# Optimization experiments

Measured on AMD Instinct MI355X. Metric: run time of the kernel, lower is better.

Reference implementation:

```python
import jax, jax.numpy as jnp
import numpy as np

B, L, D, V, O = 512, 256, 256, 100000, 1000  # L must equal D (see MaxPool1d(kernel_size=D) + squeeze)


def setup_inputs() -> dict:
    key = jax.random.key(0)
    k1, k2, k3, k4, k5 = jax.random.split(key, 5)
    input_sentence = jax.random.randint(k1, (B, L), 0, V)
    emb_weight = jax.random.normal(k2, (V, D), dtype=jnp.float32) * 0.02
    # xavier_uniform for W_b: bound = sqrt(6/(D+D))
    bound = float(np.sqrt(6.0 / (D + D)))
    W_b = jax.random.uniform(k3, (D, D), dtype=jnp.float32, minval=-bound, maxval=bound)
    lw = float(np.sqrt(1.0 / D))
    lin_w = jax.random.uniform(k4, (O, D), dtype=jnp.float32, minval=-lw, maxval=lw)
    lin_b = jax.random.uniform(k5, (O,), dtype=jnp.float32, minval=-lw, maxval=lw)
    return {"input_sentence": input_sentence, "emb_weight": emb_weight,
            "W_b": W_b, "lin_w": lin_w, "lin_b": lin_b}


def reference(input_sentence, emb_weight, W_b, lin_w, lin_b):
    # Embedding lookup: [B, L, D]
    we = emb_weight[input_sentence]
    # torch stores embeddings as [B, D, L] then re-transposes inside the co-attention;
    # net effect: C = tanh(E W_b E^T) with E = [B, L, D]  ->  C: [B, L, L]
    C = jnp.tanh(jnp.einsum('bld,de,bme->blm', we, W_b, we))
    # Dropout(p=0.5) is identity in eval mode.
    # MaxPool1d(kernel_size=D) over last axis with L == D -> max over last dim, keepdims
    max_cow = jnp.max(C, axis=-1, keepdims=True)          # [B, L, 1]
    a_q = jax.nn.softmax(max_cow, axis=1)                  # softmax over L
    # bmm(a_q^T [B,1,L], E [B,L,D]) -> [B,1,D], then squeeze dim 1
    f_w = jnp.einsum('blo,bld->bod', a_q, we)[:, 0, :]     # [B, D]
    return f_w @ lin_w.T + lin_b                           # [B, O]
```

## Files before the change

### kernel.cpp

```cpp
#include <hip/hip_runtime.h>
#include <hip/hip_bf16.h>
#include <math.h>

#define B_ 512
#define L_ 256
#define D_ 256
#define V_ 100000
#define O_ 1000

typedef __attribute__((ext_vector_type(8))) short short8;
typedef __attribute__((ext_vector_type(4))) float f32x4;

static __device__ __forceinline__ unsigned short f2bf(float f) {
    union { float f; unsigned u; } v; v.f = f;
    unsigned r = v.u + 0x7FFFu + ((v.u >> 16) & 1u);
    return (unsigned short)(r >> 16);
}
static __device__ __forceinline__ float bf2f(unsigned short u) {
    union { unsigned u; float f; } v; v.u = ((unsigned)u) << 16;
    return v.f;
}
static __device__ __forceinline__ short8 pack8(float4 a, float4 c) {
    short8 o;
    o[0] = (short)f2bf(a.x); o[1] = (short)f2bf(a.y);
    o[2] = (short)f2bf(a.z); o[3] = (short)f2bf(a.w);
    o[4] = (short)f2bf(c.x); o[5] = (short)f2bf(c.y);
    o[6] = (short)f2bf(c.z); o[7] = (short)f2bf(c.w);
    return o;
}
static __device__ __forceinline__ int fsw(int d) { return d ^ (((d >> 5) & 7) << 2); }

__global__ __launch_bounds__(256) void k_wt(const float* __restrict__ Wb,
                                            unsigned short* __restrict__ Wbf) {
    int i = blockIdx.x * 256 + threadIdx.x;
    Wbf[i] = f2bf(Wb[i]);
}

__global__ __launch_bounds__(1024, 4) void k_attn(const int* __restrict__ tok,
                                                  const float* __restrict__ emb,
                                                  const unsigned short* __restrict__ Wbf,
                                                  float* __restrict__ fw) {
    __shared__ __align__(16) char lds[163840];
    char* EsC = lds;
    float* red2    = (float*)(lds + 131072);
    float* scratch = (float*)(lds + 132096);
    float* fred    = (float*)(lds + 132160);

    int b = blockIdx.x;
    int tid = threadIdx.x;
    int wid = tid >> 6, ln = tid & 63;
    int l16 = ln & 15, gp = ln >> 4;
    int i0 = wid * 16;
    const int* tb = tok + (b << 8);

    short8 wfr[8];
#pragma unroll
    for (int k = 0; k < 8; k++)
        wfr[k] = *(const short8*)(Wbf + ((i0 + l16) << 8) + k * 32 + gp * 8);

#pragma unroll
    for (int it = 0; it < 2; it++) {
        int c = it * 1024 + tid;
        int row = c >> 5, c16 = c & 31;
        const float4* src = (const float4*)(emb + ((size_t)tb[row] << 8) + (c16 << 3));
        short8 o = pack8(src[0], src[1]);
        *(short8*)(EsC + ((row << 9) | ((c16 << 4) ^ ((row & 7) << 4)))) = o;
    }
    __syncthreads();

    float4 ga[3], gb[3];
#pragma unroll
    for (int it = 0; it < 3; it++) {
        int c = (it + 2) * 1024 + tid;
        int row = c >> 5, c16 = c & 31;
        const float4* src = (const float4*)(emb + ((size_t)tb[row] << 8) + (c16 << 3));
        ga[it] = src[0]; gb[it] = src[1];
    }

    float rmax[4];
#pragma unroll
    for (int i = 0; i < 4; i++) rmax[i] = -1e30f;

    auto P1strip = [&](int s, char* HtW) {
        f32x4 acc[2] = {};
#pragma unroll
        for (int k0 = 0; k0 < 256; k0 += 32) {
            int kk2 = (k0 + gp * 8) * 2;
            short8 b1[2];
#pragma unroll
            for (int cf = 0; cf < 2; cf++) {
                int jg = s * 32 + cf * 16 + l16;
                b1[cf] = *(const short8*)(EsC + ((jg << 9) | (kk2 ^ ((jg & 7) << 4))));
            }
            int ks = k0 >> 5;
            __builtin_amdgcn_s_setprio(1);
#pragma unroll
            for (int cf = 0; cf < 2; cf++)
                acc[cf] = __builtin_amdgcn_mfma_f32_16x16x32_bf16(
                    wfr[ks], b1[cf], acc[cf], 0, 0, 0);
            __builtin_amdgcn_s_setprio(0);
        }
#pragma unroll
        for (int cf = 0; cf < 2; cf++) {
            int i = i0 + gp * 4;
            int jl = cf * 16 + l16;
            unsigned long long pk;
            unsigned short* p = (unsigned short*)&pk;
            p[0] = f2bf(acc[cf][0]);
            p[1] = f2bf(acc[cf][1]);
            p[2] = f2bf(acc[cf][2]);
            p[3] = f2bf(acc[cf][3]);
            *(unsigned long long*)(HtW + ((jl << 9) | ((i * 2) ^ ((jl & 7) << 4)))) = pk;
        }
    };

    short8 efr[8];
    auto P2strip = [&](char* HtR) {
        f32x4 acc[2] = {};
#pragma unroll
        for (int k0 = 0; k0 < 256; k0 += 32) {
            int kk2 = (k0 + gp * 8) * 2;
            short8 b2[2];
#pragma unroll
            for (int cf = 0; cf < 2; cf++) {
                int m = cf * 16 + l16;
                b2[cf] = *(const short8*)(HtR + ((m << 9) | (kk2 ^ ((m & 7) << 4))));
            }
            int ks = k0 >> 5;
            __builtin_amdgcn_s_setprio(1);
#pragma unroll
            for (int cf = 0; cf < 2; cf++)
                acc[cf] = __builtin_amdgcn_mfma_f32_16x16x32_bf16(
                    efr[ks], b2[cf], acc[cf], 0, 0, 0);
            __builtin_amdgcn_s_setprio(0);
        }
#pragma unroll
        for (int r = 0; r < 4; r++)
            rmax[r] = fmaxf(rmax[r], fmaxf(acc[0][r], acc[1][r]));
    };

    P1strip(0, lds + 131072);

#pragma unroll
    for (int it = 0; it < 3; it++) {
        int c = (it + 2) * 1024 + tid;
        int row = c >> 5, c16 = c & 31;
        short8 o = pack8(ga[it], gb[it]);
        *(short8*)(EsC + ((row << 9) | ((c16 << 4) ^ ((row & 7) << 4)))) = o;
    }
#pragma unroll
    for (int it = 5; it < 8; it++) {
        int c = it * 1024 + tid;
        int row = c >> 5, c16 = c & 31;
        const float4* src = (const float4*)(emb + ((size_t)tb[row] << 8) + (c16 << 3));
        short8 o = pack8(src[0], src[1]);
        *(short8*)(EsC + ((row << 9) | ((c16 << 4) ^ ((row & 7) << 4)))) = o;
    }
    __syncthreads();

#pragma unroll
    for (int k = 0; k < 8; k++) {
        int l = i0 + l16;
        efr[k] = *(const short8*)(EsC + ((l << 9) | ((k * 64 + gp * 16) ^ ((l & 7) << 4))));
    }

    for (int s = 1; s < 8; s++) {
        char* HtW = lds + 131072 + ((s & 1) << 14);
        char* HtR = lds + 131072 + (((s - 1) & 1) << 14);
        f32x4 a1[2] = {};
        f32x4 a2[2] = {};
#pragma unroll
        for (int k0 = 0; k0 < 256; k0 += 32) {
            int kk2 = (k0 + gp * 8) * 2;
            short8 b1[2], b2[2];
#pragma unroll
            for (int cf = 0; cf < 2; cf++) {
                int jg = s * 32 + cf * 16 + l16;
                b1[cf] = *(const short8*)(EsC + ((jg << 9) | (kk2 ^ ((jg & 7) << 4))));
                int m = cf * 16 + l16;
                b2[cf] = *(const short8*)(HtR + ((m << 9) | (kk2 ^ ((m & 7) << 4))));
            }
            int ks = k0 >> 5;
            __builtin_amdgcn_s_setprio(1);
#pragma unroll
            for (int cf = 0; cf < 2; cf++) {
                a1[cf] = __builtin_amdgcn_mfma_f32_16x16x32_bf16(
                    wfr[ks], b1[cf], a1[cf], 0, 0, 0);
                a2[cf] = __builtin_amdgcn_mfma_f32_16x16x32_bf16(
                    efr[ks], b2[cf], a2[cf], 0, 0, 0);
            }
            __builtin_amdgcn_s_setprio(0);
        }
#pragma unroll
        for (int cf = 0; cf < 2; cf++) {
            int i = i0 + gp * 4;
            int jl = cf * 16 + l16;
            unsigned long long pk;
            unsigned short* p = (unsigned short*)&pk;
            p[0] = f2bf(a1[cf][0]);
            p[1] = f2bf(a1[cf][1]);
            p[2] = f2bf(a1[cf][2]);
            p[3] = f2bf(a1[cf][3]);
            *(unsigned long long*)(HtW + ((jl << 9) | ((i * 2) ^ ((jl & 7) << 4)))) = pk;
        }
#pragma unroll
        for (int r = 0; r < 4; r++)
            rmax[r] = fmaxf(rmax[r], fmaxf(a2[0][r], a2[1][r]));
        __syncthreads();
    }

    P2strip(lds + 131072 + (1 << 14));

#pragma unroll
    for (int i = 0; i < 4; i++) {
        float v = rmax[i];
        v = fmaxf(v, __shfl_xor(v, 1));
        v = fmaxf(v, __shfl_xor(v, 2));
        v = fmaxf(v, __shfl_xor(v, 4));
        v = fmaxf(v, __shfl_xor(v, 8));
        rmax[i] = v;
    }
    __syncthreads();
    if (l16 == 0) {
#pragma unroll
        for (int r = 0; r < 4; r++)
            red2[i0 + gp * 4 + r] = rmax[r];
    }
    __syncthreads();

    float x = -1e30f;
    if (tid < 256) x = tanhf(red2[tid]);
    float mx = x;
#pragma unroll
    for (int s = 1; s < 64; s <<= 1) mx = fmaxf(mx, __shfl_xor(mx, s));
    if (ln == 0 && wid < 4) scratch[wid] = mx;
    __syncthreads();
    float bm = fmaxf(fmaxf(scratch[0], scratch[1]), fmaxf(scratch[2], scratch[3]));
    float e = (tid < 256) ? expf(x - bm) : 0.f;
    float sm = e;
#pragma unroll
    for (int s = 1; s < 64; s <<= 1) sm += __shfl_xor(sm, s);
    if (ln == 0 && wid < 4) scratch[8 + wid] = sm;
    __syncthreads();
    float tot = (scratch[8] + scratch[9]) + (scratch[10] + scratch[11]);
    if (tid < 256) red2[tid] = e / tot;
    __syncthreads();

    if (tid < 512) {
        int g = tid >> 5;
        int d0 = (tid & 31) << 3;
        float s0[8] = {0.f, 0.f, 0.f, 0.f, 0.f, 0.f, 0.f, 0.f};
        int lbase = g << 4;
#pragma unroll
        for (int li = 0; li < 16; li++) {
            int l = lbase + li;
            float aql = red2[l];
            int byt = (l << 9) | ((d0 * 2) ^ ((l & 7) << 4));
            short8 v = *(const short8*)(EsC + byt);
#pragma unroll
            for (int jj = 0; jj < 8; jj++)
                s0[jj] += aql * bf2f((unsigned short)v[jj]);
        }
        f32x4 w0, w1;
        w0[0] = s0[0]; w0[1] = s0[1]; w0[2] = s0[2]; w0[3] = s0[3];
        w1[0] = s0[4]; w1[1] = s0[5]; w1[2] = s0[6]; w1[3] = s0[7];
        *(f32x4*)(fred + g * 256 + fsw(d0)) = w0;
        *(f32x4*)(fred + g * 256 + fsw(d0 + 4)) = w1;
    }
    __syncthreads();
    if (tid < 256) {
        float f = 0.f;
        int dw = fsw(tid);
#pragma unroll
        for (int g2 = 0; g2 < 16; g2++) f += fred[g2 * 256 + dw];
        fw[(b << 8) + tid] = f;
    }
}

__global__ __launch_bounds__(256) void k_out(const float* __restrict__ fw,
                                             const float* __restrict__ lw,
                                             const float* __restrict__ lb,
                                             float* __restrict__ out) {
    __shared__ float As[32][68];
    __shared__ float Bs[64][65];
    int tid = threadIdx.x;
    int tx = tid & 15, ty = tid >> 4;
    int r0 = blockIdx.y * 32, n0 = blockIdx.x * 64;
    float acc[2][4] = {};
    for (int k0 = 0; k0 < 256; k0 += 64) {
        __syncthreads();
#pragma unroll
        for (int it = 0; it < 2; it++) {
            int idx = it * 256 + tid;
            int i = idx >> 4, k4 = (idx & 15) << 2;
            *(float4*)&As[i][k4] = *(const float4*)&fw[(r0 + i) * 256 + k0 + k4];
        }
#pragma unroll
        for (int it = 0; it < 4; it++) {
            int idx = it * 256 + tid;
            int n = idx >> 4, k4 = (idx & 15) << 2;
            int nn = n0 + n;
            float4 v = {0.f, 0.f, 0.f, 0.f};
            if (nn < O_) v = *(const float4*)&lw[(size_t)nn * 256 + k0 + k4];
            Bs[k4][n] = v.x; Bs[k4 + 1][n] = v.y; Bs[k4 + 2][n] = v.z; Bs[k4 + 3][n] = v.w;
        }
        __syncthreads();
#pragma unroll
        for (int k = 0; k < 64; k++) {
            float a0 = As[ty * 2][k], a1 = As[ty * 2 + 1][k];
            float b0 = Bs[k][tx * 4], b1 = Bs[k][tx * 4 + 1];
            float b2 = Bs[k][tx * 4 + 2], b3 = Bs[k][tx * 4 + 3];
            acc[0][0] += a0 * b0; acc[0][1] += a0 * b1; acc[0][2] += a0 * b2; acc[0][3] += a0 * b3;
            acc[1][0] += a1 * b0; acc[1][1] += a1 * b1; acc[1][2] += a1 * b2; acc[1][3] += a1 * b3;
        }
    }
#pragma unroll
    for (int i = 0; i < 2; i++)
#pragma unroll
        for (int j = 0; j < 4; j++) {
            int n = n0 + tx * 4 + j;
            if (n < O_) out[(size_t)(r0 + ty * 2 + i) * O_ + n] = acc[i][j] + lb[n];
        }
}

extern "C" void kernel_launch(void* const* d_in, const int* in_sizes, int n_in,
                              void* d_out, int out_size, void* d_ws, size_t ws_size,
                              hipStream_t stream) {
    const int* tok = (const int*)d_in[0];
    const float* emb = (const float*)d_in[1];
    const float* Wb = (const float*)d_in[2];
    const float* lw = (const float*)d_in[3];
    const float* lb = (const float*)d_in[4];
    float* out = (float*)d_out;

    char* ws = (char*)d_ws;
    unsigned short* Wbf = (unsigned short*)(ws);
    float*          fwp = (float*)(ws + 131072);

    hipLaunchKernelGGL(k_wt,   dim3(256),    dim3(256),  0, stream, Wb, Wbf);
    hipLaunchKernelGGL(k_attn, dim3(512),    dim3(1024), 0, stream, tok, emb, Wbf, fwp);
    hipLaunchKernelGGL(k_out,  dim3(16, 16), dim3(256),  0, stream, fwp, lw, lb, out);
}
```

Baseline: 89.15 us.

## Split waves into producer and consumer roles for the two chained GEMM stages

Waves 0-7 now compute the H = W_b·E^T strips (stage 1), and waves 8-15 compute the E·H strips plus the row max (stage 2). Each wave now owns a 32-row tile instead of 16. While the producers run strip 0, the consumer waves gather the rest of the embedding rows. This is meant to overlap the two MFMA stages across waves and give each wave more register reuse. The cost is that each wave holds twice as many accumulators and fragments, so register pressure rises, and only half the waves issue MFMAs for each stage.

```diff
diff --git a/kernel.cpp b/kernel.cpp
--- a/kernel.cpp
+++ b/kernel.cpp
@@ -50,13 +50,9 @@
     int tid = threadIdx.x;
     int wid = tid >> 6, ln = tid & 63;
     int l16 = ln & 15, gp = ln >> 4;
-    int i0 = wid * 16;
+    bool prod = (wid < 8);
+    int i0 = (prod ? wid : (wid - 8)) * 32;
     const int* tb = tok + (b << 8);
-
-    short8 wfr[8];
-#pragma unroll
-    for (int k = 0; k < 8; k++)
-        wfr[k] = *(const short8*)(Wbf + ((i0 + l16) << 8) + k * 32 + gp * 8);
 
 #pragma unroll
     for (int it = 0; it < 2; it++) {
@@ -66,23 +62,23 @@
         short8 o = pack8(src[0], src[1]);
         *(short8*)(EsC + ((row << 9) | ((c16 << 4) ^ ((row & 7) << 4)))) = o;
     }
-    __syncthreads();
-
-    float4 ga[3], gb[3];
-#pragma unroll
-    for (int it = 0; it < 3; it++) {
-        int c = (it + 2) * 1024 + tid;
-        int row = c >> 5, c16 = c & 31;
-        const float4* src = (const float4*)(emb + ((size_t)tb[row] << 8) + (c16 << 3));
-        ga[it] = src[0]; gb[it] = src[1];
-    }
-
-    float rmax[4];
-#pragma unroll
-    for (int i = 0; i < 4; i++) rmax[i] = -1e30f;
+
+    short8 afr[8][2];
+    if (prod) {
+#pragma unroll
+        for (int k = 0; k < 8; k++)
+#pragma unroll
+            for (int rf = 0; rf < 2; rf++)
+                afr[k][rf] = *(const short8*)(Wbf + ((i0 + rf * 16 + l16) << 8) + k * 32 + gp * 8);
+    }
+    __syncthreads();
+
+    float rmax[8];
+#pragma unroll
+    for (int i = 0; i < 8; i++) rmax[i] = -1e30f;
 
     auto P1strip = [&](int s, char* HtW) {
-        f32x4 acc[2] = {};
+        f32x4 acc[2][2] = {};
 #pragma unroll
         for (int k0 = 0; k0 < 256; k0 += 32) {
             int kk2 = (k0 + gp * 8) * 2;
@@ -95,28 +91,31 @@
             int ks = k0 >> 5;
             __builtin_amdgcn_s_setprio(1);
 #pragma unroll
-            for (int cf = 0; cf < 2; cf++)
-                acc[cf] = __builtin_amdgcn_mfma_f32_16x16x32_bf16(
-                    wfr[ks], b1[cf], acc[cf], 0, 0, 0);
+            for (int rf = 0; rf < 2; rf++)
+#pragma unroll
+                for (int cf = 0; cf < 2; cf++)
+                    acc[rf][cf] = __builtin_amdgcn_mfma_f32_16x16x32_bf16(
+                        afr[ks][rf], b1[cf], acc[rf][cf], 0, 0, 0);
             __builtin_amdgcn_s_setprio(0);
         }
 #pragma unroll
-        for (int cf = 0; cf < 2; cf++) {
-            int i = i0 + gp * 4;
-            int jl = cf * 16 + l16;
-            unsigned long long pk;
-            unsigned short* p = (unsigned short*)&pk;
-            p[0] = f2bf(acc[cf][0]);
-            p[1] = f2bf(acc[cf][1]);
-            p[2] = f2bf(acc[cf][2]);
-            p[3] = f2bf(acc[cf][3]);
-            *(unsigned long long*)(HtW + ((jl << 9) | ((i * 2) ^ ((jl & 7) << 4)))) = pk;
-        }
+        for (int rf = 0; rf < 2; rf++)
+#pragma unroll
+            for (int cf = 0; cf < 2; cf++) {
+                int i = i0 + rf * 16 + gp * 4;
+                int jl = cf * 16 + l16;
+                unsigned long long pk;
+                unsigned short* p = (unsigned short*)&pk;
+                p[0] = f2bf(acc[rf][cf][0]);
+                p[1] = f2bf(acc[rf][cf][1]);
+                p[2] = f2bf(acc[rf][cf][2]);
+                p[3] = f2bf(acc[rf][cf][3]);
+                *(unsigned long long*)(HtW + ((jl << 9) | ((i * 2) ^ ((jl & 7) << 4)))) = pk;
+            }
     };
 
-    short8 efr[8];
     auto P2strip = [&](char* HtR) {
-        f32x4 acc[2] = {};
+        f32x4 acc[2][2] = {};
 #pragma unroll
         for (int k0 = 0; k0 < 256; k0 += 32) {
             int kk2 = (k0 + gp * 8) * 2;
@@ -129,102 +128,70 @@
             int ks = k0 >> 5;
             __builtin_amdgcn_s_setprio(1);
 #pragma unroll
-            for (int cf = 0; cf < 2; cf++)
-                acc[cf] = __builtin_amdgcn_mfma_f32_16x16x32_bf16(
-                    efr[ks], b2[cf], acc[cf], 0, 0, 0);
+            for (int rf = 0; rf < 2; rf++)
+#pragma unroll
+                for (int cf = 0; cf < 2; cf++)
+                    acc[rf][cf] = __builtin_amdgcn_mfma_f32_16x16x32_bf16(
+                        afr[ks][rf], b2[cf], acc[rf][cf], 0, 0, 0);
             __builtin_amdgcn_s_setprio(0);
         }
 #pragma unroll
-        for (int r = 0; r < 4; r++)
-            rmax[r] = fmaxf(rmax[r], fmaxf(acc[0][r], acc[1][r]));
+        for (int rf = 0; rf < 2; rf++)
+#pragma unroll
+            for (int r = 0; r < 4; r++)
+                rmax[rf * 4 + r] = fmaxf(rmax[rf * 4 + r],
+                                         fmaxf(acc[rf][0][r], acc[rf][1][r]));
     };
 
-    P1strip(0, lds + 131072);
-
-#pragma unroll
-    for (int it = 0; it < 3; it++) {
-        int c = (it + 2) * 1024 + tid;
-        int row = c >> 5, c16 = c & 31;
-        short8 o = pack8(ga[it], gb[it]);
-        *(short8*)(EsC + ((row << 9) | ((c16 << 4) ^ ((row & 7) << 4)))) = o;
-    }
-#pragma unroll
-    for (int it = 5; it < 8; it++) {
-        int c = it * 1024 + tid;
-        int row = c >> 5, c16 = c & 31;
-        const float4* src = (const float4*)(emb + ((size_t)tb[row] << 8) + (c16 << 3));
-        short8 o = pack8(src[0], src[1]);
-        *(short8*)(EsC + ((row << 9) | ((c16 << 4) ^ ((row & 7) << 4)))) = o;
-    }
-    __syncthreads();
-
-#pragma unroll
-    for (int k = 0; k < 8; k++) {
-        int l = i0 + l16;
-        efr[k] = *(const short8*)(EsC + ((l << 9) | ((k * 64 + gp * 16) ^ ((l & 7) << 4))));
+    if (prod) {
+        P1strip(0, lds + 131072);
+    } else {
+        int t4 = tid - 512;
+#pragma unroll 2
+        for (int it = 0; it < 12; it++) {
+            int c = it * 512 + t4;
+            int row = 64 + (c >> 5), c16 = c & 31;
+            const float4* src = (const float4*)(emb + ((size_t)tb[row] << 8) + (c16 << 3));
+            short8 o = pack8(src[0], src[1]);
+            *(short8*)(EsC + ((row << 9) | ((c16 << 4) ^ ((row & 7) << 4)))) = o;
+        }
+    }
+    __syncthreads();
+
+    if (!prod) {
+#pragma unroll
+        for (int k = 0; k < 8; k++)
+#pragma unroll
+            for (int rf = 0; rf < 2; rf++) {
+                int l = i0 + rf * 16 + l16;
+                afr[k][rf] = *(const short8*)(EsC +
+                    ((l << 9) | ((k * 64 + gp * 16) ^ ((l & 7) << 4))));
+            }
     }
 
     for (int s = 1; s < 8; s++) {
-        char* HtW = lds + 131072 + ((s & 1) << 14);
-        char* HtR = lds + 131072 + (((s - 1) & 1) << 14);
-        f32x4 a1[2] = {};
-        f32x4 a2[2] = {};
-#pragma unroll
-        for (int k0 = 0; k0 < 256; k0 += 32) {
-            int kk2 = (k0 + gp * 8) * 2;
-            short8 b1[2], b2[2];
-#pragma unroll
-            for (int cf = 0; cf < 2; cf++) {
-                int jg = s * 32 + cf * 16 + l16;
-                b1[cf] = *(const short8*)(EsC + ((jg << 9) | (kk2 ^ ((jg & 7) << 4))));
-                int m = cf * 16 + l16;
-                b2[cf] = *(const short8*)(HtR + ((m << 9) | (kk2 ^ ((m & 7) << 4))));
-            }
-            int ks = k0 >> 5;
-            __builtin_amdgcn_s_setprio(1);
-#pragma unroll
-            for (int cf = 0; cf < 2; cf++) {
-                a1[cf] = __builtin_amdgcn_mfma_f32_16x16x32_bf16(
-                    wfr[ks], b1[cf], a1[cf], 0, 0, 0);
-                a2[cf] = __builtin_amdgcn_mfma_f32_16x16x32_bf16(
-                    efr[ks], b2[cf], a2[cf], 0, 0, 0);
-            }
-            __builtin_amdgcn_s_setprio(0);
-        }
-#pragma unroll
-        for (int cf = 0; cf < 2; cf++) {
-            int i = i0 + gp * 4;
-            int jl = cf * 16 + l16;
-            unsigned long long pk;
-            unsigned short* p = (unsigned short*)&pk;
-            p[0] = f2bf(a1[cf][0]);
-            p[1] = f2bf(a1[cf][1]);
-            p[2] = f2bf(a1[cf][2]);
-            p[3] = f2bf(a1[cf][3]);
-            *(unsigned long long*)(HtW + ((jl << 9) | ((i * 2) ^ ((jl & 7) << 4)))) = pk;
-        }
-#pragma unroll
-        for (int r = 0; r < 4; r++)
-            rmax[r] = fmaxf(rmax[r], fmaxf(a2[0][r], a2[1][r]));
+        if (prod) P1strip(s, lds + 131072 + ((s & 1) << 14));
+        else      P2strip(lds + 131072 + (((s - 1) & 1) << 14));
         __syncthreads();
     }
-
-    P2strip(lds + 131072 + (1 << 14));
-
-#pragma unroll
-    for (int i = 0; i < 4; i++) {
-        float v = rmax[i];
-        v = fmaxf(v, __shfl_xor(v, 1));
-        v = fmaxf(v, __shfl_xor(v, 2));
-        v = fmaxf(v, __shfl_xor(v, 4));
-        v = fmaxf(v, __shfl_xor(v, 8));
-        rmax[i] = v;
-    }
-    __syncthreads();
-    if (l16 == 0) {
-#pragma unroll
-        for (int r = 0; r < 4; r++)
-            red2[i0 + gp * 4 + r] = rmax[r];
+    if (!prod) {
+        P2strip(lds + 131072 + (1 << 14));
+#pragma unroll
+        for (int i = 0; i < 8; i++) {
+            float v = rmax[i];
+            v = fmaxf(v, __shfl_xor(v, 1));
+            v = fmaxf(v, __shfl_xor(v, 2));
+            v = fmaxf(v, __shfl_xor(v, 4));
+            v = fmaxf(v, __shfl_xor(v, 8));
+            rmax[i] = v;
+        }
+        if (l16 == 0) {
+#pragma unroll
+            for (int rf = 0; rf < 2; rf++)
+#pragma unroll
+                for (int r = 0; r < 4; r++)
+                    red2[i0 + rf * 16 + gp * 4 + r] = rmax[rf * 4 + r];
+        }
     }
     __syncthreads();
 
```

Result: faster. 81.26 us (-8.8%).
